# Performance work log

Hardware: AMD Instinct MI355X
Metric: run time of the kernel (lower is better)

The kernel has to match this reference:

```python
import jax, jax.numpy as jnp
import numpy as np

B, C1, C2 = 8, 256, 256
Cc = 128          # c = int(c2 * e)
RED = 16          # reduction in FrequencyModulation
HEADS = 8
HD = Cc // HEADS  # 16
HH, WW = 32, 32


def _c1x1(x, w, b=None):
    # 1x1 conv as channel contraction; w: [out_c, in_c]
    y = jnp.einsum('bchw,oc->bohw', x, w)
    return y if b is None else y + b[None, :, None, None]


def setup_inputs() -> dict:
    key = jax.random.key(0)
    ks = jax.random.split(key, 22)
    s = 0.02
    p = {}
    p['x'] = jax.random.normal(ks[0], (B, C1, HH, WW), jnp.float32)
    p['cv1_w'] = jax.random.normal(ks[1], (2 * Cc, C1), jnp.float32) * s
    p['cv1_b'] = jnp.zeros((2 * Cc,), jnp.float32)
    # FrequencyModulation params
    p['fm_w1'] = jax.random.normal(ks[2], (Cc // RED, Cc), jnp.float32) * s
    p['fm_w2'] = jax.random.normal(ks[3], (Cc, Cc // RED), jnp.float32) * s
    p['ca_w1'] = jax.random.normal(ks[4], (Cc // RED, Cc), jnp.float32) * s
    p['ca_w2'] = jax.random.normal(ks[5], (Cc, Cc // RED), jnp.float32) * s
    # TokenStatisticsSelfAttention params (qkv_bias=False)
    p['qkv_w'] = jax.random.normal(ks[6], (3 * Cc, Cc), jnp.float32) * s
    p['tproj_w'] = jax.random.normal(ks[7], (Cc, Cc), jnp.float32) * s
    p['tproj_b'] = jnp.zeros((Cc,), jnp.float32)
    # SpatialQuantizedRouter params
    p['dw_w'] = jax.random.normal(ks[8], (Cc, 1, 3, 3), jnp.float32) * s  # depthwise
    p['dw_b'] = jnp.zeros((Cc,), jnp.float32)
    p['rt_w'] = jax.random.normal(ks[9], (1, Cc), jnp.float32) * s
    p['rt_b'] = jnp.zeros((1,), jnp.float32)
    p['q_w'] = jax.random.normal(ks[10], (Cc, Cc), jnp.float32) * s
    p['k_w'] = jax.random.normal(ks[11], (Cc, Cc), jnp.float32) * s
    p['v_w'] = jax.random.normal(ks[12], (Cc, Cc), jnp.float32) * s
    p['sproj_w'] = jax.random.normal(ks[13], (Cc, Cc), jnp.float32) * s
    p['sproj_b'] = jnp.zeros((Cc,), jnp.float32)
    p['cv2_w'] = jax.random.normal(ks[14], (C2, 3 * Cc), jnp.float32) * s
    p['cv2_b'] = jnp.zeros((C2,), jnp.float32)
    return p


def _forward(x, cv1_w, cv1_b, fm_w1, fm_w2, ca_w1, ca_w2, qkv_w, tproj_w,
             tproj_b, dw_w, dw_b, rt_w, rt_b, q_w, k_w, v_w, sproj_w,
             sproj_b, cv2_w, cv2_b):
    Bb, _, H, W = x.shape
    N = H * W
    y = _c1x1(x, cv1_w, cv1_b)
    y0, y1 = y[:, :Cc], y[:, Cc:]

    # ---- Branch 1: FrequencyModulation ----
    xf = jnp.fft.rfft2(y1.astype(jnp.float32), norm='ortho')  # [B,c,H,W//2+1] complex
    mag = jnp.abs(xf)
    pooled = mag.mean(axis=(-2, -1))                          # [B,c]
    fw = jax.nn.sigmoid(jax.nn.relu(pooled @ fm_w1.T) @ fm_w2.T)  # [B,c]
    # mag*fw*exp(i*phase) == fw * xf  (fw is real, per batch/channel)
    xs = jnp.fft.irfft2(xf * fw[:, :, None, None].astype(jnp.complex64),
                        s=(H, W), norm='ortho')               # [B,c,H,W]
    ca = jax.nn.sigmoid(jax.nn.relu(xs.mean(axis=(-2, -1)) @ ca_w1.T) @ ca_w2.T)
    freq_out = xs * ca[:, :, None, None]

    # ---- Branch 2: TokenStatisticsSelfAttention ----
    xt = y1.reshape(Bb, Cc, N).transpose(0, 2, 1)             # [B,N,c]
    qkv = (xt @ qkv_w.T).reshape(Bb, N, 3, HEADS, HD).transpose(2, 0, 3, 1, 4)
    q, k, v = qkv[0], qkv[1], qkv[2]                          # [B,h,N,d]
    var_v = jnp.var(v, axis=-1, ddof=1, keepdims=True)        # [B,h,N,1] (unbiased)
    var_k = jnp.var(k, axis=-1, ddof=1, keepdims=True)
    attn = jax.nn.softmax(jnp.einsum('bhnx,bhmx->bhnm', var_v, var_k) * (HD ** -0.5), axis=-1)
    to = jnp.einsum('bhnm,bhmd->bhnd', attn, v).transpose(0, 2, 1, 3).reshape(Bb, N, Cc)
    stat_out = ((to @ tproj_w.T) + tproj_b).transpose(0, 2, 1).reshape(Bb, Cc, H, W)

    # ---- Branch 3: SpatialQuantizedRouter (training-mode blend) ----
    x_local = jax.lax.conv_general_dilated(
        y1, dw_w, (1, 1), 'SAME', feature_group_count=Cc,
        dimension_numbers=('NCHW', 'OIHW', 'NCHW')) + dw_b[None, :, None, None]
    p_route = jax.nn.sigmoid(y1.mean(axis=(-2, -1)) @ rt_w.T + rt_b)  # [B,1]
    qb = jnp.sign(_c1x1(y1, q_w).reshape(Bb, Cc, N))
    kb = jnp.sign(_c1x1(y1, k_w).reshape(Bb, Cc, N))
    vv = _c1x1(y1, v_w).reshape(Bb, Cc, N)
    a2 = jax.nn.softmax(jnp.einsum('bcn,bcm->bnm', qb, kb) * (Cc ** -0.5), axis=-1)
    # torch: bmm(v, attn.T) -> out[b,c,n] = sum_m v[b,c,m]*attn[b,n,m]
    ob = jnp.einsum('bcm,bnm->bcn', vv, a2).reshape(Bb, Cc, H, W)
    out_bin = _c1x1(ob, sproj_w, sproj_b)
    alpha = p_route.reshape(Bb, 1, 1, 1)
    spat_out = (1.0 - alpha) * x_local + alpha * out_bin

    attn_out = freq_out + stat_out + spat_out
    yc = jnp.concatenate([y0, y1, attn_out], axis=1)          # [B,3c,H,W]
    out = _c1x1(yc, cv2_w, cv2_b)
    return x + out  # add: shortcut and c1 == c2


def reference(x, cv1_w, cv1_b, fm_w1, fm_w2, ca_w1, ca_w2, qkv_w, tproj_w,
              tproj_b, dw_w, dw_b, rt_w, rt_b, q_w, k_w, v_w, sproj_w,
              sproj_b, cv2_w, cv2_b):
    return _forward(x, cv1_w, cv1_b, fm_w1, fm_w2, ca_w1, ca_w2, qkv_w,
                    tproj_w, tproj_b, dw_w, dw_b, rt_w, rt_b, q_w, k_w, v_w,
                    sproj_w, sproj_b, cv2_w, cv2_b)
```

## Files before the change

### kernel.cpp

```cpp
#include <hip/hip_runtime.h>
#include <math.h>

#define BATCH 8
#define NPIX 1024

typedef __attribute__((ext_vector_type(8))) short short8v;
typedef __attribute__((ext_vector_type(4))) float f32x4;

__device__ inline unsigned short f2bf(float x) {
  unsigned int u = __float_as_uint(x);
  return (unsigned short)((u + 0x7FFFu + ((u >> 16) & 1u)) >> 16);
}
__device__ inline float bf2f(unsigned short h) {
  return __uint_as_float((unsigned int)h << 16);
}
__device__ inline unsigned long long pack4bf(float a, float b, float c, float d) {
  return (unsigned long long)(unsigned short)f2bf(a) |
         ((unsigned long long)(unsigned short)f2bf(b) << 16) |
         ((unsigned long long)(unsigned short)f2bf(c) << 32) |
         ((unsigned long long)(unsigned short)f2bf(d) << 48);
}

__global__ __launch_bounds__(256) void convw_kernel(
    const float* __restrict__ cv1_w, const float* __restrict__ qkv_w,
    const float* __restrict__ tproj_w, const float* __restrict__ sproj_w,
    const float* __restrict__ cv2_w, const float* __restrict__ q_w,
    const float* __restrict__ k_w, const float* __restrict__ v_w,
    short* __restrict__ wb) {
  int i = blockIdx.x * 256 + threadIdx.x;
  float v;
  if (i < 65536) v = cv1_w[i];
  else if (i < 163840) {
    int j = i - 65536;
    if (j < 49152) v = qkv_w[j];
    else {
      int jj = j - 49152, wsel = jj >> 14, r = jj & 16383;
      v = (wsel == 0) ? q_w[r] : (wsel == 1) ? k_w[r] : v_w[r];
    }
  }
  else if (i < 180224) v = tproj_w[i - 163840];
  else if (i < 196608) v = sproj_w[i - 180224];
  else v = cv2_w[i - 196608];
  wb[i] = (short)f2bf(v);
}

__global__ __launch_bounds__(256) void tconv_kernel(
    const float* __restrict__ src, long sSrc, int dstStride, int dstOff,
    short* __restrict__ dst) {
  __shared__ float t[64][65];
  const int b = blockIdx.z;
  const int c0 = blockIdx.x * 64, n0 = blockIdx.y * 64;
  const float* s = src + (long)b * sSrc;
  short* d = dst + (long)b * 1024 * dstStride;
  const int tid = threadIdx.x;
#pragma unroll
  for (int p = 0; p < 16; p++) {
    int idx = tid + p * 256;
    int cl = idx >> 6, nl = idx & 63;
    t[cl][nl] = s[(long)(c0 + cl) * 1024 + n0 + nl];
  }
  __syncthreads();
#pragma unroll
  for (int p = 0; p < 16; p++) {
    int idx = tid + p * 256;
    int nl = idx >> 6, cl = idx & 63;
    d[(long)(n0 + nl) * dstStride + dstOff + c0 + cl] = (short)f2bf(t[cl][nl]);
  }
}

template<int MODE, bool HAS_BIAS, bool HAS_RES>
__global__ __launch_bounds__(256) void mgemm_kernel(
    const short* __restrict__ Wb, const short* __restrict__ XT, int ldx,
    const float* __restrict__ bias, const float* __restrict__ res,
    void* __restrict__ Y0, void* __restrict__ Y1,
    int K, long sXT, long sY, long sR) {
  __shared__ __align__(16) short As[64][40];
  __shared__ __align__(16) short Bs[64][40];
  const int b = blockIdx.z;
  const int n0 = blockIdx.x * 64, m0 = blockIdx.y * 64;
  const int tid = threadIdx.x;
  const int l = tid & 63, w = tid >> 6;
  const int wm = w >> 1, wn = w & 1;
  const short* Xb = XT + (long)b * sXT;
  const int sr = tid >> 2, sko = (tid & 3) * 8;
  const int fr = l & 15, fk = (l >> 4) * 8;
  f32x4 acc[2][2] = {};
  for (int k0 = 0; k0 < K; k0 += 32) {
    *(uint4*)&As[sr][sko] = *(const uint4*)(Wb + (long)(m0 + sr) * K + k0 + sko);
    *(uint4*)&Bs[sr][sko] = *(const uint4*)(Xb + (long)(n0 + sr) * ldx + k0 + sko);
    __syncthreads();
    short8v a0 = *(short8v*)&As[wm * 32 + fr][fk];
    short8v a1 = *(short8v*)&As[wm * 32 + 16 + fr][fk];
    short8v b0 = *(short8v*)&Bs[wn * 32 + fr][fk];
    short8v b1 = *(short8v*)&Bs[wn * 32 + 16 + fr][fk];
    acc[0][0] = __builtin_amdgcn_mfma_f32_16x16x32_bf16(a0, b0, acc[0][0], 0, 0, 0);
    acc[0][1] = __builtin_amdgcn_mfma_f32_16x16x32_bf16(a0, b1, acc[0][1], 0, 0, 0);
    acc[1][0] = __builtin_amdgcn_mfma_f32_16x16x32_bf16(a1, b0, acc[1][0], 0, 0, 0);
    acc[1][1] = __builtin_amdgcn_mfma_f32_16x16x32_bf16(a1, b1, acc[1][1], 0, 0, 0);
    __syncthreads();
  }
#pragma unroll
  for (int tm = 0; tm < 2; tm++) {
    const int m_base = m0 + wm * 32 + tm * 16 + (l >> 4) * 4;
#pragma unroll
    for (int tn = 0; tn < 2; tn++) {
      const int n = n0 + wn * 32 + tn * 16 + (l & 15);
      float v0 = acc[tm][tn][0], v1 = acc[tm][tn][1];
      float v2 = acc[tm][tn][2], v3 = acc[tm][tn][3];
      if (HAS_BIAS) {
        v0 += bias[m_base]; v1 += bias[m_base + 1];
        v2 += bias[m_base + 2]; v3 += bias[m_base + 3];
      }
      if (MODE == 0 || MODE == 1) {
        if (HAS_RES) {
          v0 += res[(long)b * sR + (long)(m_base + 0) * 1024 + n];
          v1 += res[(long)b * sR + (long)(m_base + 1) * 1024 + n];
          v2 += res[(long)b * sR + (long)(m_base + 2) * 1024 + n];
          v3 += res[(long)b * sR + (long)(m_base + 3) * 1024 + n];
        }
        if (MODE == 0) {
          float* Y = (float*)Y0 + (long)b * sY + n;
          Y[(long)(m_base + 0) * 1024] = v0; Y[(long)(m_base + 1) * 1024] = v1;
          Y[(long)(m_base + 2) * 1024] = v2; Y[(long)(m_base + 3) * 1024] = v3;
        } else {
          short* Y = (short*)Y0 + (long)b * sY + n;
          Y[(long)(m_base + 0) * 1024] = (short)f2bf(v0);
          Y[(long)(m_base + 1) * 1024] = (short)f2bf(v1);
          Y[(long)(m_base + 2) * 1024] = (short)f2bf(v2);
          Y[(long)(m_base + 3) * 1024] = (short)f2bf(v3);
        }
      } else if (MODE == 2) {
        *(unsigned long long*)((short*)Y0 + ((long)b * 1024 + n) * 384 + m_base) =
            pack4bf(v0, v1, v2, v3);
        if (m_base >= 128) {
          float* Y = (float*)Y1 + ((long)b * 128 + m_base - 128) * 1024 + n;
          Y[0] = v0; Y[1024] = v1; Y[2048] = v2; Y[3072] = v3;
        }
      } else {
        if (m0 < 384) {
          float* Y = (float*)Y0 + (long)b * 384 * 1024 + (long)m_base * 1024 + n;
          Y[0] = v0; Y[1024] = v1; Y[2048] = v2; Y[3072] = v3;
        } else {
          *(unsigned long long*)((short*)Y1 + ((long)b * 1024 + n) * 384 +
                                 (m_base - 384)) = pack4bf(v0, v1, v2, v3);
        }
      }
    }
  }
}

__global__ __launch_bounds__(256) void fftpool_kernel(
    const float* __restrict__ y1, float* __restrict__ pooled, float* __restrict__ m1) {
  const int bc = blockIdx.x;
  const float* img = y1 + (long)bc * NPIX;
  __shared__ float im[1024];
  __shared__ float Gr[32][17], Gi[32][17];
  __shared__ float cs[32], sn[32];
  __shared__ float red[256];
  const int t = threadIdx.x;
  if (t < 32) {
    float ang = -0.19634954084936207f * (float)t;
    __sincosf(ang, &sn[t], &cs[t]);
  }
  float lsum = 0.f;
  for (int i = t; i < 1024; i += 256) { float v = img[i]; im[i] = v; lsum += v; }
  red[t] = lsum;
  __syncthreads();
  for (int s = 128; s > 0; s >>= 1) {
    if (t < s) red[t] += red[t + s];
    __syncthreads();
  }
  if (t == 0) m1[bc] = red[0] * (1.f / 1024.f);
  for (int i = t; i < 544; i += 256) {
    int h = i / 17, v = i % 17;
    float ar = 0.f, ai = 0.f;
    for (int w2 = 0; w2 < 32; w2++) {
      int k = (v * w2) & 31;
      float x = im[h * 32 + w2];
      ar += x * cs[k]; ai += x * sn[k];
    }
    Gr[h][v] = ar; Gi[h][v] = ai;
  }
  __syncthreads();
  float asum = 0.f;
  for (int i = t; i < 544; i += 256) {
    int u = i / 17, v = i % 17;
    float xr = 0.f, xi = 0.f;
    for (int h = 0; h < 32; h++) {
      int k = (u * h) & 31;
      float gr = Gr[h][v], gi = Gi[h][v];
      xr += gr * cs[k] - gi * sn[k];
      xi += gr * sn[k] + gi * cs[k];
    }
    asum += sqrtf(xr * xr + xi * xi);
  }
  red[t] = asum;
  __syncthreads();
  for (int s = 128; s > 0; s >>= 1) {
    if (t < s) red[t] += red[t + s];
    __syncthreads();
  }
  if (t == 0) pooled[bc] = red[0] * (1.f / (32.f * 544.f));
}

__global__ __launch_bounds__(128) void gates_kernel(
    const float* __restrict__ pooled, const float* __restrict__ m1,
    const float* __restrict__ fm_w1, const float* __restrict__ fm_w2,
    const float* __restrict__ ca_w1, const float* __restrict__ ca_w2,
    const float* __restrict__ rt_w, const float* __restrict__ rt_b,
    float* __restrict__ g, float* __restrict__ alpha) {
  const int b = blockIdx.x, t = threadIdx.x;
  __shared__ float h1[8], fwv[128], xsm[128], h2[8];
  const float* pb = pooled + b * 128;
  const float* mb = m1 + b * 128;
  if (t < 8) {
    float s = 0.f;
    for (int c = 0; c < 128; c++) s += pb[c] * fm_w1[t * 128 + c];
    h1[t] = fmaxf(s, 0.f);
  }
  __syncthreads();
  {
    float s = 0.f;
    for (int r = 0; r < 8; r++) s += h1[r] * fm_w2[t * 8 + r];
    float fw = 1.f / (1.f + __expf(-s));
    fwv[t] = fw; xsm[t] = fw * mb[t];
  }
  __syncthreads();
  if (t < 8) {
    float s = 0.f;
    for (int c = 0; c < 128; c++) s += xsm[c] * ca_w1[t * 128 + c];
    h2[t] = fmaxf(s, 0.f);
  }
  __syncthreads();
  {
    float s = 0.f;
    for (int r = 0; r < 8; r++) s += h2[r] * ca_w2[t * 8 + r];
    float ca = 1.f / (1.f + __expf(-s));
    g[b * 128 + t] = fwv[t] * ca;
  }
  if (t == 0) {
    float s = 0.f;
    for (int c = 0; c < 128; c++) s += mb[c] * rt_w[c];
    s += rt_b[0];
    alpha[b] = 1.f / (1.f + __expf(-s));
  }
}

__global__ __launch_bounds__(256) void varmax_kernel(
    const float* __restrict__ qkvb, float* __restrict__ var_k,
    float* __restrict__ var_v, float* __restrict__ maxvk,
    short* __restrict__ vTb) {
  const int bh = blockIdx.x;
  const int b = bh >> 3, h = bh & 7;
  __shared__ float red[256];
  __shared__ float trans[16][256];
  const float* kb = qkvb + ((long)b * 384 + 128 + h * 16) * NPIX;
  const float* vb = qkvb + ((long)b * 384 + 256 + h * 16) * NPIX;
  float mx = 0.f;
  for (int j = 0; j < 4; j++) {
    int n = threadIdx.x + j * 256;
    float xk[16], xv[16], sk = 0.f, sv = 0.f;
#pragma unroll
    for (int d = 0; d < 16; d++) {
      xk[d] = kb[(long)d * NPIX + n]; sk += xk[d];
      xv[d] = vb[(long)d * NPIX + n]; sv += xv[d];
    }
    float mk = sk * (1.f / 16.f), mv = sv * (1.f / 16.f);
    float vk_ = 0.f, vv_ = 0.f;
#pragma unroll
    for (int d = 0; d < 16; d++) {
      float a = xk[d] - mk; vk_ += a * a;
      float c = xv[d] - mv; vv_ += c * c;
    }
    vk_ *= (1.f / 15.f); vv_ *= (1.f / 15.f);
    var_k[(long)bh * NPIX + n] = vk_;
    var_v[(long)bh * NPIX + n] = vv_;
    mx = fmaxf(mx, vk_);
#pragma unroll
    for (int d = 0; d < 16; d++) trans[d][threadIdx.x] = xv[d];
    __syncthreads();
    {
      int d = threadIdx.x >> 4, mc = threadIdx.x & 15;
      __align__(16) short tmp[16];
#pragma unroll
      for (int e = 0; e < 16; e++) tmp[e] = (short)f2bf(trans[d][mc * 16 + e]);
      short* dst = vTb + ((long)bh * 16 + d) * 1024 + j * 256 + mc * 16;
      *(uint4*)dst = *(uint4*)tmp;
      *(uint4*)(dst + 8) = *(uint4*)(tmp + 8);
    }
    __syncthreads();
  }
  red[threadIdx.x] = mx;
  __syncthreads();
  for (int s = 128; s > 0; s >>= 1) {
    if (threadIdx.x < s) red[threadIdx.x] = fmaxf(red[threadIdx.x], red[threadIdx.x + s]);
    __syncthreads();
  }
  if (threadIdx.x == 0) maxvk[bh] = red[0];
}

__global__ __launch_bounds__(256) void stat_mfma_kernel(
    const short* __restrict__ vTb, const float* __restrict__ var_k,
    const float* __restrict__ var_v, const float* __restrict__ maxvk,
    short* __restrict__ tcT) {
  const int bh = blockIdx.x;
  const int b = bh >> 3, h = bh & 7;
  const int n0 = blockIdx.y * 64;
  const int tid = threadIdx.x;
  const int l = tid & 63, w = tid >> 6;
  const int ln = l & 15, lk = l >> 4;
  const int n = n0 + w * 16 + ln;
  __shared__ float vk[1024];
  for (int i = tid; i < 1024; i += 256) vk[i] = var_k[(long)bh * 1024 + i];
  const float cn = var_v[(long)bh * 1024 + n] * 0.25f;
  const float mv = maxvk[bh];
  const short* arow = vTb + ((long)bh * 16 + ln) * 1024 + lk * 8;
  __syncthreads();
  f32x4 acc = {};
  float psum = 0.f;
  for (int m0 = 0; m0 < 1024; m0 += 32) {
    short8v afrag = *(const short8v*)(arow + m0);
    short8v bfrag;
#pragma unroll
    for (int j = 0; j < 8; j++) {
      float wv = __expf(cn * (vk[m0 + lk * 8 + j] - mv));
      psum += wv;
      bfrag[j] = (short)f2bf(wv);
    }
    acc = __builtin_amdgcn_mfma_f32_16x16x32_bf16(afrag, bfrag, acc, 0, 0, 0);
  }
  psum += __shfl_xor(psum, 16);
  psum += __shfl_xor(psum, 32);
  const float inv = 1.f / psum;
  *(unsigned long long*)(tcT + ((long)b * 1024 + n) * 128 + h * 16 + lk * 4) =
      pack4bf(acc[0] * inv, acc[1] * inv, acc[2] * inv, acc[3] * inv);
}

__global__ __launch_bounds__(256) void pack_kernel(
    const short* __restrict__ sqkvT,
    unsigned long long* __restrict__ qbits, unsigned long long* __restrict__ kbits) {
  const int wave = threadIdx.x >> 6, lane = threadIdx.x & 63;
  const long p = (long)blockIdx.x * 4 + wave;
  const short* base = sqkvT + p * 384;
  unsigned long long q0 = __ballot(bf2f((unsigned short)base[lane]) > 0.f);
  unsigned long long q1 = __ballot(bf2f((unsigned short)base[64 + lane]) > 0.f);
  unsigned long long k0 = __ballot(bf2f((unsigned short)base[128 + lane]) > 0.f);
  unsigned long long k1 = __ballot(bf2f((unsigned short)base[192 + lane]) > 0.f);
  if (lane == 0) {
    qbits[p * 2] = q0; qbits[p * 2 + 1] = q1;
    kbits[p * 2] = k0; kbits[p * 2 + 1] = k1;
  }
}

__global__ __launch_bounds__(256) void obgemm_kernel(
    const short* __restrict__ pvb, const unsigned long long* __restrict__ qbits,
    const unsigned long long* __restrict__ kbits, float* __restrict__ pnum,
    float* __restrict__ pden) {
  const int b = blockIdx.z;
  const int sp = blockIdx.y;
  const int n0 = blockIdx.x * 64;
  const int kb0 = sp * 256;
  __shared__ __align__(16) short As[128][40];
  __shared__ __align__(16) unsigned long long kbsh[256][2];
  const int tid = threadIdx.x;
  const int l = tid & 63, w = tid >> 6;
  const int ln = l & 15, lk = l >> 4;
  const int n = n0 + w * 16 + ln;
  const unsigned long long q0 = qbits[((long)b * 1024 + n) * 2];
  const unsigned long long q1 = qbits[((long)b * 1024 + n) * 2 + 1];
  *(uint4*)&kbsh[tid][0] = *(const uint4*)(kbits + ((long)b * 1024 + kb0 + tid) * 2);
  const float fs = 0.08838834764831845f;
  const int sc = tid >> 1, sh = (tid & 1) * 16;
  const short* pvrow = pvb + ((long)b * 128 + sc) * 1024 + kb0;
  f32x4 acc[8] = {};
  float psum = 0.f;
  for (int ks = 0; ks < 8; ks++) {
    *(uint4*)&As[sc][sh] = *(const uint4*)(pvrow + ks * 32 + sh);
    *(uint4*)&As[sc][sh + 8] = *(const uint4*)(pvrow + ks * 32 + sh + 8);
    __syncthreads();
    const int mloc = ks * 32 + lk * 8;
    short8v bfrag;
#pragma unroll
    for (int j = 0; j < 8; j++) {
      unsigned long long kw0 = kbsh[mloc + j][0];
      unsigned long long kw1 = kbsh[mloc + j][1];
      int ham = __popcll(kw0 ^ q0) + __popcll(kw1 ^ q1);
      float wv = __expf((float)(128 - 2 * ham) * fs);
      psum += wv;
      bfrag[j] = (short)f2bf(wv);
    }
#pragma unroll
    for (int ct = 0; ct < 8; ct++) {
      short8v afrag = *(short8v*)&As[ct * 16 + ln][lk * 8];
      acc[ct] = __builtin_amdgcn_mfma_f32_16x16x32_bf16(afrag, bfrag, acc[ct], 0, 0, 0);
    }
    __syncthreads();
  }
  float* dst = pnum + (((long)sp * 8 + b) * 128) * 1024 + n;
#pragma unroll
  for (int ct = 0; ct < 8; ct++)
#pragma unroll
    for (int i = 0; i < 4; i++)
      dst[(long)(ct * 16 + lk * 4 + i) * 1024] = acc[ct][i];
  psum += __shfl_xor(psum, 16);
  psum += __shfl_xor(psum, 32);
  if (lk == 0)
    pden[((long)sp * 8 + b) * 1024 + n] = psum;
}

__global__ __launch_bounds__(256) void dwcombine_kernel(
    const float* __restrict__ y1, float* __restrict__ attn,
    const float* __restrict__ dw_w, const float* __restrict__ dw_b,
    const float* __restrict__ pnum, const float* __restrict__ pden,
    const float* __restrict__ sproj_b, const float* __restrict__ g,
    const float* __restrict__ alpha) {
  const int bc = blockIdx.x;
  const int b = bc >> 7, cx = bc & 127;
  const float* img = y1 + (long)bc * NPIX;
  float* dst = attn + (long)bc * NPIX;
  float w[9];
#pragma unroll
  for (int i = 0; i < 9; i++) w[i] = dw_w[cx * 9 + i];
  const float bias = dw_b[cx];
  const float a = alpha[b];
  const float gg = g[bc];
  const float sb = sproj_b[cx];
  const long ns = 8L * 128 * 1024;
  const long ds = 8L * 1024;
  const long nbase = (long)bc * 1024;
  const long dbase = (long)b * 1024;
  for (int i = threadIdx.x; i < 1024; i += 256) {
    int h = i >> 5, wx = i & 31;
    float s = bias;
#pragma unroll
    for (int ky = 0; ky < 3; ky++) {
      int hh = h + ky - 1;
      if (hh < 0 || hh > 31) continue;
#pragma unroll
      for (int kx = 0; kx < 3; kx++) {
        int ww2 = wx + kx - 1;
        if (ww2 < 0 || ww2 > 31) continue;
        s += img[hh * 32 + ww2] * w[ky * 3 + kx];
      }
    }
    float num = pnum[nbase + i] + pnum[nbase + i + ns] +
                pnum[nbase + i + 2 * ns] + pnum[nbase + i + 3 * ns];
    float den = pden[dbase + i] + pden[dbase + i + ds] +
                pden[dbase + i + 2 * ds] + pden[dbase + i + 3 * ds];
    float obv = num / den + sb;
    dst[i] = dst[i] + gg * img[i] + (1.f - a) * s + a * obv;
  }
}

extern "C" void kernel_launch(void* const* d_in, const int* in_sizes, int n_in,
                              void* d_out, int out_size, void* d_ws, size_t ws_size,
                              hipStream_t stream) {
  const float* x = (const float*)d_in[0];
  const float* cv1_w = (const float*)d_in[1];
  const float* cv1_b = (const float*)d_in[2];
  const float* fm_w1 = (const float*)d_in[3];
  const float* fm_w2 = (const float*)d_in[4];
  const float* ca_w1 = (const float*)d_in[5];
  const float* ca_w2 = (const float*)d_in[6];
  const float* qkv_w = (const float*)d_in[7];
  const float* tproj_w = (const float*)d_in[8];
  const float* tproj_b = (const float*)d_in[9];
  const float* dw_w = (const float*)d_in[10];
  const float* dw_b = (const float*)d_in[11];
  const float* rt_w = (const float*)d_in[12];
  const float* rt_b = (const float*)d_in[13];
  const float* q_w = (const float*)d_in[14];
  const float* k_w = (const float*)d_in[15];
  const float* v_w = (const float*)d_in[16];
  const float* sproj_w = (const float*)d_in[17];
  const float* sproj_b = (const float*)d_in[18];
  const float* cv2_w = (const float*)d_in[19];
  const float* cv2_b = (const float*)d_in[20];
  float* out = (float*)d_out;

  char* wsp = (char*)d_ws;
  size_t off = 0;
  auto alloc = [&](size_t bytes) {
    void* p = wsp + off;
    off += (bytes + 255) & ~(size_t)255;
    return p;
  };
  float* qkvb = (float*)alloc(8UL * 384 * 1024 * 4);
  float* pn_t = (float*)alloc(8UL * 128 * 1024 * 4);
  float* y1 = (float*)alloc(8UL * 128 * 1024 * 4);
  float* attn = (float*)alloc(8UL * 128 * 1024 * 4);
  short* ycT = (short*)alloc(8UL * 1024 * 384 * 2);
  short* sqkvT = (short*)alloc(8UL * 1024 * 384 * 2);
  short* xT = (short*)alloc(8UL * 1024 * 256 * 2);
  short* tcT = (short*)alloc(8UL * 1024 * 128 * 2);
  short* pvb = (short*)alloc(8UL * 128 * 1024 * 2);
  short* wb = (short*)alloc(294912UL * 2);
  short* vTb = (short*)alloc(64UL * 16 * 1024 * 2);
  float* pden = (float*)alloc(4UL * 8 * 1024 * 4);
  float* var_k = (float*)alloc(8UL * 8 * 1024 * 4);
  float* var_v = (float*)alloc(8UL * 8 * 1024 * 4);
  float* maxvk = (float*)alloc(64 * 4);
  float* pooled = (float*)alloc(1024 * 4);
  float* m1 = (float*)alloc(1024 * 4);
  float* g = (float*)alloc(1024 * 4);
  float* alpha = (float*)alloc(8 * 4);
  unsigned long long* qbits = (unsigned long long*)alloc(8192UL * 2 * 8);
  unsigned long long* kbits = (unsigned long long*)alloc(8192UL * 2 * 8);
  (void)pn_t;
  float* pnum = qkvb;
  const short* cv1b = wb;
  const short* qsb = wb + 65536;
  const short* tprojb = wb + 163840;
  const short* sprojb = wb + 180224;
  const short* cv2b = wb + 196608;
  if (off > ws_size) return;

  dim3 blk(256);
  convw_kernel<<<dim3(1152), blk, 0, stream>>>(cv1_w, qkv_w, tproj_w, sproj_w,
                                               cv2_w, q_w, k_w, v_w, wb);
  tconv_kernel<<<dim3(4, 16, 8), blk, 0, stream>>>(x, 256L * 1024, 256, 0, xT);
  mgemm_kernel<2, true, false><<<dim3(16, 4, 8), blk, 0, stream>>>(
      cv1b, xT, 256, cv1_b, nullptr, ycT, y1, 256, 1024L * 256, 0, 0);
  fftpool_kernel<<<dim3(1024), blk, 0, stream>>>(y1, pooled, m1);
  gates_kernel<<<dim3(8), dim3(128), 0, stream>>>(pooled, m1, fm_w1, fm_w2,
                                                  ca_w1, ca_w2, rt_w, rt_b, g, alpha);
  mgemm_kernel<3, false, false><<<dim3(16, 12, 8), blk, 0, stream>>>(
      qsb, ycT + 128, 384, nullptr, nullptr, qkvb, sqkvT, 128, 1024L * 384, 0, 0);
  varmax_kernel<<<dim3(64), blk, 0, stream>>>(qkvb, var_k, var_v, maxvk, vTb);
  stat_mfma_kernel<<<dim3(64, 16), blk, 0, stream>>>(vTb, var_k, var_v, maxvk, tcT);
  mgemm_kernel<0, true, false><<<dim3(16, 2, 8), blk, 0, stream>>>(
      tprojb, tcT, 128, tproj_b, nullptr, attn, nullptr, 128, 1024L * 128,
      128L * 1024, 0);
  pack_kernel<<<dim3(2048), blk, 0, stream>>>(sqkvT, qbits, kbits);
  mgemm_kernel<1, false, false><<<dim3(16, 2, 8), blk, 0, stream>>>(
      sprojb, sqkvT + 256, 384, nullptr, nullptr, pvb, nullptr, 128,
      1024L * 384, 128L * 1024, 0);
  obgemm_kernel<<<dim3(16, 4, 8), blk, 0, stream>>>(pvb, qbits, kbits, pnum, pden);
  dwcombine_kernel<<<dim3(1024), blk, 0, stream>>>(y1, attn, dw_w, dw_b, pnum,
                                                   pden, sproj_b, g, alpha);
  tconv_kernel<<<dim3(2, 16, 8), blk, 0, stream>>>(attn, 128L * 1024, 384, 256, ycT);
  mgemm_kernel<0, true, true><<<dim3(16, 4, 8), blk, 0, stream>>>(
      cv2b, ycT, 384, cv2_b, x, out, nullptr, 384, 1024L * 384, 256L * 1024,
      256L * 1024);
}
```

Before: 125.9 us.

## Fuse transposes into GEMM loads/epilogues, reorder tproj GEMM, store pnum as bf16

Removes both tconv_kernel launches. The cv1 GEMM now reads fp32 x directly and transposes and converts it to bf16 while staging into shared memory. The tproj GEMM moves after dwcombine, adds attn as a residual and writes transposed bf16 straight into ycT, so dwcombine no longer reads attn back. The obgemm partial numerators are stored as bf16 to halve that traffic. In exchange the B-tile staging uses scalar, strided shared-memory stores that may cause bank conflicts, and bf16 partial sums lose some precision.

```diff
diff --git a/kernel.cpp b/kernel.cpp
--- a/kernel.cpp
+++ b/kernel.cpp
@@ -44,36 +44,12 @@
   wb[i] = (short)f2bf(v);
 }
 
-__global__ __launch_bounds__(256) void tconv_kernel(
-    const float* __restrict__ src, long sSrc, int dstStride, int dstOff,
-    short* __restrict__ dst) {
-  __shared__ float t[64][65];
-  const int b = blockIdx.z;
-  const int c0 = blockIdx.x * 64, n0 = blockIdx.y * 64;
-  const float* s = src + (long)b * sSrc;
-  short* d = dst + (long)b * 1024 * dstStride;
-  const int tid = threadIdx.x;
-#pragma unroll
-  for (int p = 0; p < 16; p++) {
-    int idx = tid + p * 256;
-    int cl = idx >> 6, nl = idx & 63;
-    t[cl][nl] = s[(long)(c0 + cl) * 1024 + n0 + nl];
-  }
-  __syncthreads();
-#pragma unroll
-  for (int p = 0; p < 16; p++) {
-    int idx = tid + p * 256;
-    int nl = idx >> 6, cl = idx & 63;
-    d[(long)(n0 + nl) * dstStride + dstOff + c0 + cl] = (short)f2bf(t[cl][nl]);
-  }
-}
-
-template<int MODE, bool HAS_BIAS, bool HAS_RES>
+template<int MODE, bool HAS_BIAS, bool HAS_RES, bool XF32T, bool EMIT_HI>
 __global__ __launch_bounds__(256) void mgemm_kernel(
-    const short* __restrict__ Wb, const short* __restrict__ XT, int ldx,
+    const short* __restrict__ Wb, const void* __restrict__ Xsrc, int ldx,
     const float* __restrict__ bias, const float* __restrict__ res,
     void* __restrict__ Y0, void* __restrict__ Y1,
-    int K, long sXT, long sY, long sR) {
+    int K, long sXT, long sY, long sR, int tStride, int tOff) {
   __shared__ __align__(16) short As[64][40];
   __shared__ __align__(16) short Bs[64][40];
   const int b = blockIdx.z;
@@ -81,13 +57,24 @@
   const int tid = threadIdx.x;
   const int l = tid & 63, w = tid >> 6;
   const int wm = w >> 1, wn = w & 1;
-  const short* Xb = XT + (long)b * sXT;
   const int sr = tid >> 2, sko = (tid & 3) * 8;
+  const int xr = tid >> 3, xcg = (tid & 7) * 8;
   const int fr = l & 15, fk = (l >> 4) * 8;
   f32x4 acc[2][2] = {};
   for (int k0 = 0; k0 < K; k0 += 32) {
     *(uint4*)&As[sr][sko] = *(const uint4*)(Wb + (long)(m0 + sr) * K + k0 + sko);
-    *(uint4*)&Bs[sr][sko] = *(const uint4*)(Xb + (long)(n0 + sr) * ldx + k0 + sko);
+    if (XF32T) {
+      const float* Xf = (const float*)Xsrc + (long)b * sXT;
+      const float4 xa = *(const float4*)(Xf + (long)(k0 + xr) * 1024 + n0 + xcg);
+      const float4 xb = *(const float4*)(Xf + (long)(k0 + xr) * 1024 + n0 + xcg + 4);
+      Bs[xcg + 0][xr] = (short)f2bf(xa.x); Bs[xcg + 1][xr] = (short)f2bf(xa.y);
+      Bs[xcg + 2][xr] = (short)f2bf(xa.z); Bs[xcg + 3][xr] = (short)f2bf(xa.w);
+      Bs[xcg + 4][xr] = (short)f2bf(xb.x); Bs[xcg + 5][xr] = (short)f2bf(xb.y);
+      Bs[xcg + 6][xr] = (short)f2bf(xb.z); Bs[xcg + 7][xr] = (short)f2bf(xb.w);
+    } else {
+      const short* Xb = (const short*)Xsrc + (long)b * sXT;
+      *(uint4*)&Bs[sr][sko] = *(const uint4*)(Xb + (long)(n0 + sr) * ldx + k0 + sko);
+    }
     __syncthreads();
     short8v a0 = *(short8v*)&As[wm * 32 + fr][fk];
     short8v a1 = *(short8v*)&As[wm * 32 + 16 + fr][fk];
@@ -111,28 +98,26 @@
         v0 += bias[m_base]; v1 += bias[m_base + 1];
         v2 += bias[m_base + 2]; v3 += bias[m_base + 3];
       }
-      if (MODE == 0 || MODE == 1) {
-        if (HAS_RES) {
-          v0 += res[(long)b * sR + (long)(m_base + 0) * 1024 + n];
-          v1 += res[(long)b * sR + (long)(m_base + 1) * 1024 + n];
-          v2 += res[(long)b * sR + (long)(m_base + 2) * 1024 + n];
-          v3 += res[(long)b * sR + (long)(m_base + 3) * 1024 + n];
-        }
-        if (MODE == 0) {
-          float* Y = (float*)Y0 + (long)b * sY + n;
-          Y[(long)(m_base + 0) * 1024] = v0; Y[(long)(m_base + 1) * 1024] = v1;
-          Y[(long)(m_base + 2) * 1024] = v2; Y[(long)(m_base + 3) * 1024] = v3;
-        } else {
-          short* Y = (short*)Y0 + (long)b * sY + n;
-          Y[(long)(m_base + 0) * 1024] = (short)f2bf(v0);
-          Y[(long)(m_base + 1) * 1024] = (short)f2bf(v1);
-          Y[(long)(m_base + 2) * 1024] = (short)f2bf(v2);
-          Y[(long)(m_base + 3) * 1024] = (short)f2bf(v3);
-        }
+      if (HAS_RES) {
+        v0 += res[(long)b * sR + (long)(m_base + 0) * 1024 + n];
+        v1 += res[(long)b * sR + (long)(m_base + 1) * 1024 + n];
+        v2 += res[(long)b * sR + (long)(m_base + 2) * 1024 + n];
+        v3 += res[(long)b * sR + (long)(m_base + 3) * 1024 + n];
+      }
+      if (MODE == 0) {
+        float* Y = (float*)Y0 + (long)b * sY + n;
+        Y[(long)(m_base + 0) * 1024] = v0; Y[(long)(m_base + 1) * 1024] = v1;
+        Y[(long)(m_base + 2) * 1024] = v2; Y[(long)(m_base + 3) * 1024] = v3;
+      } else if (MODE == 1) {
+        short* Y = (short*)Y0 + (long)b * sY + n;
+        Y[(long)(m_base + 0) * 1024] = (short)f2bf(v0);
+        Y[(long)(m_base + 1) * 1024] = (short)f2bf(v1);
+        Y[(long)(m_base + 2) * 1024] = (short)f2bf(v2);
+        Y[(long)(m_base + 3) * 1024] = (short)f2bf(v3);
       } else if (MODE == 2) {
-        *(unsigned long long*)((short*)Y0 + ((long)b * 1024 + n) * 384 + m_base) =
-            pack4bf(v0, v1, v2, v3);
-        if (m_base >= 128) {
+        *(unsigned long long*)((short*)Y0 + ((long)b * 1024 + n) * tStride +
+                               tOff + m_base) = pack4bf(v0, v1, v2, v3);
+        if (EMIT_HI && m_base >= 128) {
           float* Y = (float*)Y1 + ((long)b * 128 + m_base - 128) * 1024 + n;
           Y[0] = v0; Y[1024] = v1; Y[2048] = v2; Y[3072] = v3;
         }
@@ -354,7 +339,7 @@
 
 __global__ __launch_bounds__(256) void obgemm_kernel(
     const short* __restrict__ pvb, const unsigned long long* __restrict__ qbits,
-    const unsigned long long* __restrict__ kbits, float* __restrict__ pnum,
+    const unsigned long long* __restrict__ kbits, short* __restrict__ pnum,
     float* __restrict__ pden) {
   const int b = blockIdx.z;
   const int sp = blockIdx.y;
@@ -396,12 +381,12 @@
     }
     __syncthreads();
   }
-  float* dst = pnum + (((long)sp * 8 + b) * 128) * 1024 + n;
+  short* dst = pnum + (((long)sp * 8 + b) * 128) * 1024 + n;
 #pragma unroll
   for (int ct = 0; ct < 8; ct++)
 #pragma unroll
     for (int i = 0; i < 4; i++)
-      dst[(long)(ct * 16 + lk * 4 + i) * 1024] = acc[ct][i];
+      dst[(long)(ct * 16 + lk * 4 + i) * 1024] = (short)f2bf(acc[ct][i]);
   psum += __shfl_xor(psum, 16);
   psum += __shfl_xor(psum, 32);
   if (lk == 0)
@@ -411,7 +396,7 @@
 __global__ __launch_bounds__(256) void dwcombine_kernel(
     const float* __restrict__ y1, float* __restrict__ attn,
     const float* __restrict__ dw_w, const float* __restrict__ dw_b,
-    const float* __restrict__ pnum, const float* __restrict__ pden,
+    const short* __restrict__ pnum, const float* __restrict__ pden,
     const float* __restrict__ sproj_b, const float* __restrict__ g,
     const float* __restrict__ alpha) {
   const int bc = blockIdx.x;
@@ -443,12 +428,14 @@
         s += img[hh * 32 + ww2] * w[ky * 3 + kx];
       }
     }
-    float num = pnum[nbase + i] + pnum[nbase + i + ns] +
-                pnum[nbase + i + 2 * ns] + pnum[nbase + i + 3 * ns];
+    float num = bf2f((unsigned short)pnum[nbase + i]) +
+                bf2f((unsigned short)pnum[nbase + i + ns]) +
+                bf2f((unsigned short)pnum[nbase + i + 2 * ns]) +
+                bf2f((unsigned short)pnum[nbase + i + 3 * ns]);
     float den = pden[dbase + i] + pden[dbase + i + ds] +
                 pden[dbase + i + 2 * ds] + pden[dbase + i + 3 * ds];
     float obv = num / den + sb;
-    dst[i] = dst[i] + gg * img[i] + (1.f - a) * s + a * obv;
+    dst[i] = gg * img[i] + (1.f - a) * s + a * obv;
   }
 }
 
@@ -486,12 +473,10 @@
     return p;
   };
   float* qkvb = (float*)alloc(8UL * 384 * 1024 * 4);
-  float* pn_t = (float*)alloc(8UL * 128 * 1024 * 4);
   float* y1 = (float*)alloc(8UL * 128 * 1024 * 4);
   float* attn = (float*)alloc(8UL * 128 * 1024 * 4);
   short* ycT = (short*)alloc(8UL * 1024 * 384 * 2);
   short* sqkvT = (short*)alloc(8UL * 1024 * 384 * 2);
-  short* xT = (short*)alloc(8UL * 1024 * 256 * 2);
   short* tcT = (short*)alloc(8UL * 1024 * 128 * 2);
   short* pvb = (short*)alloc(8UL * 128 * 1024 * 2);
   short* wb = (short*)alloc(294912UL * 2);
@@ -506,8 +491,7 @@
   float* alpha = (float*)alloc(8 * 4);
   unsigned long long* qbits = (unsigned long long*)alloc(8192UL * 2 * 8);
   unsigned long long* kbits = (unsigned long long*)alloc(8192UL * 2 * 8);
-  (void)pn_t;
-  float* pnum = qkvb;
+  short* pnum = (short*)qkvb;
   const short* cv1b = wb;
   const short* qsb = wb + 65536;
   const short* tprojb = wb + 163840;
@@ -518,28 +502,27 @@
   dim3 blk(256);
   convw_kernel<<<dim3(1152), blk, 0, stream>>>(cv1_w, qkv_w, tproj_w, sproj_w,
                                                cv2_w, q_w, k_w, v_w, wb);
-  tconv_kernel<<<dim3(4, 16, 8), blk, 0, stream>>>(x, 256L * 1024, 256, 0, xT);
-  mgemm_kernel<2, true, false><<<dim3(16, 4, 8), blk, 0, stream>>>(
-      cv1b, xT, 256, cv1_b, nullptr, ycT, y1, 256, 1024L * 256, 0, 0);
+  mgemm_kernel<2, true, false, true, true><<<dim3(16, 4, 8), blk, 0, stream>>>(
+      cv1b, x, 0, cv1_b, nullptr, ycT, y1, 256, 256L * 1024, 0, 0, 384, 0);
   fftpool_kernel<<<dim3(1024), blk, 0, stream>>>(y1, pooled, m1);
   gates_kernel<<<dim3(8), dim3(128), 0, stream>>>(pooled, m1, fm_w1, fm_w2,
                                                   ca_w1, ca_w2, rt_w, rt_b, g, alpha);
-  mgemm_kernel<3, false, false><<<dim3(16, 12, 8), blk, 0, stream>>>(
-      qsb, ycT + 128, 384, nullptr, nullptr, qkvb, sqkvT, 128, 1024L * 384, 0, 0);
+  mgemm_kernel<3, false, false, false, false><<<dim3(16, 12, 8), blk, 0, stream>>>(
+      qsb, ycT + 128, 384, nullptr, nullptr, qkvb, sqkvT, 128, 1024L * 384,
+      0, 0, 0, 0);
   varmax_kernel<<<dim3(64), blk, 0, stream>>>(qkvb, var_k, var_v, maxvk, vTb);
   stat_mfma_kernel<<<dim3(64, 16), blk, 0, stream>>>(vTb, var_k, var_v, maxvk, tcT);
-  mgemm_kernel<0, true, false><<<dim3(16, 2, 8), blk, 0, stream>>>(
-      tprojb, tcT, 128, tproj_b, nullptr, attn, nullptr, 128, 1024L * 128,
-      128L * 1024, 0);
   pack_kernel<<<dim3(2048), blk, 0, stream>>>(sqkvT, qbits, kbits);
-  mgemm_kernel<1, false, false><<<dim3(16, 2, 8), blk, 0, stream>>>(
+  mgemm_kernel<1, false, false, false, false><<<dim3(16, 2, 8), blk, 0, stream>>>(
       sprojb, sqkvT + 256, 384, nullptr, nullptr, pvb, nullptr, 128,
-      1024L * 384, 128L * 1024, 0);
+      1024L * 384, 128L * 1024, 0, 0, 0);
   obgemm_kernel<<<dim3(16, 4, 8), blk, 0, stream>>>(pvb, qbits, kbits, pnum, pden);
   dwcombine_kernel<<<dim3(1024), blk, 0, stream>>>(y1, attn, dw_w, dw_b, pnum,
                                                    pden, sproj_b, g, alpha);
-  tconv_kernel<<<dim3(2, 16, 8), blk, 0, stream>>>(attn, 128L * 1024, 384, 256, ycT);
-  mgemm_kernel<0, true, true><<<dim3(16, 4, 8), blk, 0, stream>>>(
+  mgemm_kernel<2, true, true, false, false><<<dim3(16, 2, 8), blk, 0, stream>>>(
+      tprojb, tcT, 128, tproj_b, attn, ycT, nullptr, 128, 1024L * 128, 0,
+      128L * 1024, 384, 256);
+  mgemm_kernel<0, true, true, false, false><<<dim3(16, 4, 8), blk, 0, stream>>>(
       cv2b, ycT, 384, cv2_b, x, out, nullptr, 384, 1024L * 384, 256L * 1024,
-      256L * 1024);
-}
+      256L * 1024, 0, 0);
+}
```

Result: faster. 123.0 us (-2.3%).
